# Kernel optimization log

Hardware: AMD Instinct MI355X
Metric: run time of the kernel (lower is better)

## Reference

```python
import jax, jax.numpy as jnp
import numpy as np

B, N, D, H = 16, 512, 256, 8
DK = D // H
EPS = 1e-6
NEG_INF = 1e12
LAM_ATT, LAM_DIST, LAM_ADJ = 0.3, 0.3, 0.4


def setup_inputs() -> dict:
    key = jax.random.key(0)
    ks = jax.random.split(key, 16)
    inp = {
        "query": jax.random.normal(ks[0], (B, N, D), jnp.float32),
        "key": jax.random.normal(ks[1], (B, N, D), jnp.float32),
        "value": jax.random.normal(ks[2], (B, N, D), jnp.float32),
        "adj_matrix": jax.random.uniform(ks[3], (B, N, N), jnp.float32),
        "distances_matrix": jax.random.uniform(ks[4], (B, N, N), jnp.float32),
        "edges_att": jnp.zeros((1,), jnp.float32),
        "mask": jnp.ones((B, N), jnp.int32),
    }
    s = 1.0 / np.sqrt(D)
    # four Linear(d_model, d_model): Wq, Wk, Wv, Wo (+ biases)
    for i, nm in enumerate(["q", "k", "v", "o"]):
        inp[f"W{nm}"] = jax.random.normal(ks[5 + 2 * i], (D, D), jnp.float32) * s
        inp[f"b{nm}"] = jax.random.normal(ks[6 + 2 * i], (D,), jnp.float32) * s
    return inp


def _proj(x, W, b):
    # [B,N,D] -> [B,H,N,DK]
    y = x @ W.T + b
    return y.reshape(B, N, H, DK).transpose(0, 2, 1, 3)


def reference(query, key, value, adj_matrix, distances_matrix, edges_att, mask,
              Wq, bq, Wk, bk, Wv, bv, Wo, bo):
    q = _proj(query, Wq, bq)
    k = _proj(key, Wk, bk)
    v = _proj(value, Wv, bv)

    valid = mask != 0  # [B,N] key-side validity

    # distance kernel: softmax(-d) over keys, masked positions -> 0 prob
    d_scores = jnp.where(valid[:, None, :], -distances_matrix, -jnp.inf)
    p_dist = jax.nn.softmax(d_scores, axis=-1)  # [B,N,N]

    # scaled dot-product attention with key mask
    scores = jnp.einsum("bhqd,bhkd->bhqk", q, k) / np.sqrt(DK)
    scores = jnp.where(valid[:, None, None, :], scores, -NEG_INF)
    p_attn = jax.nn.softmax(scores, axis=-1)  # [B,H,N,N]

    # row-normalized adjacency
    p_adj = adj_matrix / (adj_matrix.sum(axis=-1, keepdims=True) + EPS)  # [B,N,N]

    # blend three attention terms (broadcast dist/adj over heads)
    p_weighted = (LAM_ATT * p_attn
                  + LAM_DIST * p_dist[:, None]
                  + LAM_ADJ * p_adj[:, None])  # [B,H,N,N]

    x = jnp.einsum("bhqk,bhkd->bhqd", p_weighted, v)  # [B,H,N,DK]
    x = x.transpose(0, 2, 1, 3).reshape(B, N, D)
    out = x @ Wo.T + bo  # output projection (4th linear)
    return out
```

## Files before the change

### kernel.cpp

```cpp
#include <hip/hip_runtime.h>
#include <cstdint>
#include <cstddef>

#define B_  16
#define N_  512
#define D_  256
#define H_  8
#define DK_ 32

#define QKV_ELEMS 2097152

__device__ __align__(16) unsigned short g_Qb[QKV_ELEMS];
__device__ __align__(16) unsigned short g_Kb[QKV_ELEMS];
__device__ __align__(16) unsigned short g_VT[QKV_ELEMS];
__device__ __align__(16) unsigned short g_WqB[D_*D_];
__device__ __align__(16) unsigned short g_WkB[D_*D_];
__device__ __align__(16) unsigned short g_WvB[D_*D_];
__device__ __align__(16) unsigned short g_WoB[D_*D_];
__device__ __align__(16) unsigned short g_ST[B_*N_*N_];

typedef short v8s __attribute__((ext_vector_type(8)));
typedef float v4f __attribute__((ext_vector_type(4)));

__device__ __forceinline__ unsigned short f2b(float f){
  unsigned int x;
  __builtin_memcpy(&x, &f, 4);
  x = x + 0x7FFFu + ((x >> 16) & 1u);
  return (unsigned short)(x >> 16);
}
__device__ __forceinline__ v8s pack8(const float4 a, const float4 b){
  v8s o;
  o[0]=(short)f2b(a.x); o[1]=(short)f2b(a.y); o[2]=(short)f2b(a.z); o[3]=(short)f2b(a.w);
  o[4]=(short)f2b(b.x); o[5]=(short)f2b(b.y); o[6]=(short)f2b(b.z); o[7]=(short)f2b(b.w);
  return o;
}

__global__ __launch_bounds__(256) void prep_w(
    const float* __restrict__ Wq, const float* __restrict__ Wk,
    const float* __restrict__ Wv, const float* __restrict__ Wo)
{
  const int bid = blockIdx.x;
  const int z = bid >> 6;
  const int i = ((bid & 63)*256 + (int)threadIdx.x)*4;
  const float* src = (z==0)?Wq:(z==1)?Wk:(z==2)?Wv:Wo;
  const float4 u = *reinterpret_cast<const float4*>(src + i);
  ushort4 o4;
  o4.x = f2b(u.x); o4.y = f2b(u.y); o4.z = f2b(u.z); o4.w = f2b(u.w);
  if (z < 3){
    unsigned short* dst = (z==0)?g_WqB:(z==1)?g_WkB:g_WvB;
    *reinterpret_cast<ushort4*>(dst + i) = o4;
  } else {
    const int n = i >> 8, k = i & 255;
    *reinterpret_cast<ushort4*>(g_WoB + ((size_t)(k >> 5))*8192 + (size_t)n*32 + (k & 31)) = o4;
  }
}

__global__ __launch_bounds__(512) void qkv_st_kernel(
    const float* __restrict__ query, const float* __restrict__ key_,
    const float* __restrict__ value, const float* __restrict__ dist,
    const float* __restrict__ adjm,  const int* __restrict__ mask,
    const float* __restrict__ bq, const float* __restrict__ bk,
    const float* __restrict__ bv)
{
  const int bid = blockIdx.x;
  const int b = bid & 15, qt = bid >> 4, q0 = qt*16;
  const int t = threadIdx.x;
  const int w = t >> 6, lane = t & 63, kl = lane & 15, quad = lane >> 4;

  {
    const int row = t >> 5, seg = t & 31;
    const size_t roff = ((size_t)(b*N_ + q0 + row))*N_ + seg*16;
    const float* dp = dist + roff;
    const float* ap = adjm + roff;
    const int*   mp = mask + b*N_ + seg*16;
    float ev[16], av[16];
    float lz = 0.f, la = 0.f;
    #pragma unroll
    for (int c = 0; c < 4; ++c){
      const float4 d4 = *reinterpret_cast<const float4*>(dp + c*4);
      const float4 a4 = *reinterpret_cast<const float4*>(ap + c*4);
      const int4   m4 = *reinterpret_cast<const int4*>(mp + c*4);
      ev[c*4+0] = m4.x ? __expf(-d4.x) : 0.f;
      ev[c*4+1] = m4.y ? __expf(-d4.y) : 0.f;
      ev[c*4+2] = m4.z ? __expf(-d4.z) : 0.f;
      ev[c*4+3] = m4.w ? __expf(-d4.w) : 0.f;
      av[c*4+0]=a4.x; av[c*4+1]=a4.y; av[c*4+2]=a4.z; av[c*4+3]=a4.w;
      lz += ev[c*4+0]+ev[c*4+1]+ev[c*4+2]+ev[c*4+3];
      la += a4.x+a4.y+a4.z+a4.w;
    }
    #pragma unroll
    for (int o = 1; o < 32; o <<= 1){
      lz += __shfl_xor(lz, o, 64);
      la += __shfl_xor(la, o, 64);
    }
    const float c0 = (lz > 0.f) ? 0.3f / lz : 0.f;
    const float c1 = 0.4f / (la + 1e-6f);
    v8s s0, s1;
    #pragma unroll
    for (int i = 0; i < 8; ++i){
      s0[i] = (short)f2b(ev[i]*c0   + av[i]*c1);
      s1[i] = (short)f2b(ev[8+i]*c0 + av[8+i]*c1);
    }
    *reinterpret_cast<v8s*>(g_ST + roff)     = s0;
    *reinterpret_cast<v8s*>(g_ST + roff + 8) = s1;
  }

  {
    const size_t arow = ((size_t)(b*N_ + q0 + kl))*256;
    const int n0 = w*32;
    const v4f vz = {0.f,0.f,0.f,0.f};
    #pragma unroll
    for (int z = 0; z < 3; ++z){
      const float* Ap = (z==0)?query:(z==1)?key_:value;
      const unsigned short* WB = (z==0)?g_WqB:(z==1)?g_WkB:g_WvB;
      const float* bp = (z==0)?bq:(z==1)?bk:bv;
      v4f a0 = vz, a1 = vz;
      #pragma unroll
      for (int k0 = 0; k0 < 256; k0 += 32){
        const float* app = Ap + arow + k0 + quad*8;
        const v8s af = pack8(reinterpret_cast<const float4*>(app)[0],
                             reinterpret_cast<const float4*>(app)[1]);
        const v8s wf0 = *reinterpret_cast<const v8s*>(WB + ((size_t)(n0+kl))*256 + k0 + quad*8);
        const v8s wf1 = *reinterpret_cast<const v8s*>(WB + ((size_t)(n0+16+kl))*256 + k0 + quad*8);
        if (z < 2){
          a0 = __builtin_amdgcn_mfma_f32_16x16x32_bf16(wf0, af, a0, 0, 0, 0);
          a1 = __builtin_amdgcn_mfma_f32_16x16x32_bf16(wf1, af, a1, 0, 0, 0);
        } else {
          a0 = __builtin_amdgcn_mfma_f32_16x16x32_bf16(af, wf0, a0, 0, 0, 0);
          a1 = __builtin_amdgcn_mfma_f32_16x16x32_bf16(af, wf1, a1, 0, 0, 0);
        }
      }
      if (z < 2){
        unsigned short* dst = (z==0) ? g_Qb : g_Kb;
        #pragma unroll
        for (int nb = 0; nb < 2; ++nb){
          const v4f a = nb ? a1 : a0;
          const int nn = n0 + nb*16 + quad*4;
          const float4 b4 = *reinterpret_cast<const float4*>(bp + nn);
          ushort4 o4;
          o4.x=f2b(a[0]+b4.x); o4.y=f2b(a[1]+b4.y); o4.z=f2b(a[2]+b4.z); o4.w=f2b(a[3]+b4.w);
          *reinterpret_cast<ushort4*>(dst + (((size_t)(b*H_+w))*N_ + q0 + kl)*DK_ + (nn & 31)) = o4;
        }
      } else {
        #pragma unroll
        for (int nb = 0; nb < 2; ++nb){
          const v4f a = nb ? a1 : a0;
          const float bias = bp[n0 + nb*16 + kl];
          ushort4 o4;
          o4.x=f2b(a[0]+bias); o4.y=f2b(a[1]+bias); o4.z=f2b(a[2]+bias); o4.w=f2b(a[3]+bias);
          *reinterpret_cast<ushort4*>(g_VT + (((size_t)(b*H_+w))*16 + (qt>>1))*1024
              + (size_t)(nb*16+kl)*32 + (qt&1)*16 + quad*4) = o4;
        }
      }
    }
  }
}

__global__ __launch_bounds__(512, 4) void attn_kernel(
    const int* __restrict__ mask, const float* __restrict__ bo,
    float* __restrict__ out)
{
  __shared__ unsigned short STl[16*520];
  __shared__ unsigned short Pl[8*16*40];
  __shared__ unsigned short Xl[16*272];
  const int bid = blockIdx.x;
  const int b  = bid & 15;
  const int qt = bid >> 4;
  const int q0 = qt*16;
  const int t  = threadIdx.x;
  const int w  = t >> 6, lane = t & 63;
  const int kl = lane & 15, quad = lane >> 4;

  {
    const int row = t >> 5;
    const int c16 = (t & 31) * 16;
    const unsigned short* src = g_ST + ((size_t)(b*N_ + q0 + row))*N_ + c16;
    *reinterpret_cast<v8s*>(&STl[row*520 + c16])     = *reinterpret_cast<const v8s*>(src);
    *reinterpret_cast<v8s*>(&STl[row*520 + c16 + 8]) = *reinterpret_cast<const v8s*>(src + 8);
  }

  const int h = w;
  const size_t bh = (size_t)b*H_ + h;
  const float scale = 0.17677669529663687f;
  const unsigned short* Qp = g_Qb + (bh*N_ + q0)*DK_;
  const unsigned short* Kp = g_Kb + bh*N_*DK_;
  const unsigned short* Vp = g_VT + bh*(size_t)(N_*DK_);
  unsigned short* Plw = Pl + w*640;
  const int* mrow = mask + b*N_;
  const v8s aq = *reinterpret_cast<const v8s*>(Qp + (size_t)kl*DK_ + quad*8);
  const v4f vz = {0.f, 0.f, 0.f, 0.f};

  v4f oA0 = vz, oA1 = vz;
  v4f oS0 = vz, oS1 = vz;
  float lsum[4] = {0.f, 0.f, 0.f, 0.f};

  __syncthreads();

  #pragma unroll 1
  for (int ch = 0; ch < 4; ++ch){
    const int k0 = ch*128;
    v4f acc[8];
    #pragma unroll
    for (int kb = 0; kb < 8; ++kb){
      const v8s bk = *reinterpret_cast<const v8s*>(Kp + (size_t)(k0 + kb*16 + kl)*DK_ + quad*8);
      acc[kb] = __builtin_amdgcn_mfma_f32_16x16x32_bf16(aq, bk, vz, 0, 0, 0);
    }
    #pragma unroll
    for (int kb = 0; kb < 8; ++kb){
      const bool valid = (mrow[k0 + kb*16 + kl] != 0);
      #pragma unroll
      for (int r = 0; r < 4; ++r){
        const float e = valid ? __expf(acc[kb][r]*scale) : 0.f;
        acc[kb][r] = e;
        lsum[r] += e;
      }
    }
    #pragma unroll
    for (int cc = 0; cc < 4; ++cc){
      #pragma unroll
      for (int r = 0; r < 4; ++r){
        Plw[(quad*4 + r)*40 + kl]      = f2b(acc[2*cc    ][r]);
        Plw[(quad*4 + r)*40 + 16 + kl] = f2b(acc[2*cc + 1][r]);
      }
      const int kk = k0 + cc*32;
      const v8s bp  = *reinterpret_cast<const v8s*>(&Plw[kl*40 + quad*8]);
      const v8s bst = *reinterpret_cast<const v8s*>(&STl[kl*520 + kk + quad*8]);
      const v8s av0 = *reinterpret_cast<const v8s*>(Vp + (size_t)(kk + kl)*32 + quad*8);
      const v8s av1 = *reinterpret_cast<const v8s*>(Vp + (size_t)(kk + 16 + kl)*32 + quad*8);
      oA0 = __builtin_amdgcn_mfma_f32_16x16x32_bf16(av0, bp,  oA0, 0, 0, 0);
      oS0 = __builtin_amdgcn_mfma_f32_16x16x32_bf16(av0, bst, oS0, 0, 0, 0);
      oA1 = __builtin_amdgcn_mfma_f32_16x16x32_bf16(av1, bp,  oA1, 0, 0, 0);
      oS1 = __builtin_amdgcn_mfma_f32_16x16x32_bf16(av1, bst, oS1, 0, 0, 0);
    }
  }

  #pragma unroll
  for (int r = 0; r < 4; ++r)
    #pragma unroll
    for (int o = 1; o < 16; o <<= 1) lsum[r] += __shfl_xor(lsum[r], o, 64);
  const float s01 = (kl & 1) ? lsum[1] : lsum[0];
  const float s23 = (kl & 1) ? lsum[3] : lsum[2];
  const float sv  = (kl & 2) ? s23 : s01;
  float inv = __shfl(sv, ((kl >> 2) << 4) | (kl & 3), 64);
  inv = (inv > 0.f) ? 0.3f / inv : 0.f;

  unsigned short* xr = Xl + kl*272 + h*32;
  #pragma unroll
  for (int r = 0; r < 4; ++r){
    xr[     quad*4 + r] = f2b(oA0[r]*inv + oS0[r]);
    xr[16 + quad*4 + r] = f2b(oA1[r]*inv + oS1[r]);
  }
  __syncthreads();

  {
    const int n0 = w*32;
    v4f a2[2];
    a2[0] = vz; a2[1] = vz;
    #pragma unroll
    for (int k0 = 0; k0 < 256; k0 += 32){
      const v8s af = *reinterpret_cast<const v8s*>(&Xl[kl*272 + k0 + quad*8]);
      #pragma unroll
      for (int nb = 0; nb < 2; ++nb){
        const v8s wf = *reinterpret_cast<const v8s*>(
            g_WoB + (size_t)(k0 >> 5)*8192 + (size_t)(n0 + nb*16 + kl)*32 + quad*8);
        a2[nb] = __builtin_amdgcn_mfma_f32_16x16x32_bf16(af, wf, a2[nb], 0, 0, 0);
      }
    }
    #pragma unroll
    for (int nb = 0; nb < 2; ++nb){
      const int n = n0 + nb*16 + kl;
      const float bias = bo[n];
      #pragma unroll
      for (int r = 0; r < 4; ++r)
        out[((size_t)(b*N_ + q0 + quad*4 + r))*256 + n] = a2[nb][r] + bias;
    }
  }
}

extern "C" void kernel_launch(void* const* d_in, const int* in_sizes, int n_in,
                              void* d_out, int out_size, void* d_ws, size_t ws_size,
                              hipStream_t stream)
{
  const float* query = (const float*)d_in[0];
  const float* key_  = (const float*)d_in[1];
  const float* value = (const float*)d_in[2];
  const float* adjm  = (const float*)d_in[3];
  const float* dist  = (const float*)d_in[4];
  const int*   mask  = (const int*)d_in[6];
  const float* Wq = (const float*)d_in[7];  const float* bq = (const float*)d_in[8];
  const float* Wk = (const float*)d_in[9];  const float* bk = (const float*)d_in[10];
  const float* Wv = (const float*)d_in[11]; const float* bv = (const float*)d_in[12];
  const float* Wo = (const float*)d_in[13]; const float* bo = (const float*)d_in[14];

  prep_w<<<256, 256, 0, stream>>>(Wq, Wk, Wv, Wo);
  qkv_st_kernel<<<512, 512, 0, stream>>>(query, key_, value, dist, adjm, mask,
                                         bq, bk, bv);
  attn_kernel<<<512, 512, 0, stream>>>(mask, bo, (float*)d_out);
}
```

Before: 190.1 us.

## Split pre-kernel into separate ST and QKV projection blocks with interleaved loads

The combined kernel is split so even blocks compute the blended distance/adjacency matrix and odd blocks compute the Q/K/V projections, doubling the grid to 1024 blocks. The projection loop now issues all Q, K and V loads up front per k-step and runs six independent MFMA chains instead of three sequential passes. The ST path also hoists all its global loads before the exp work. The aim is more parallelism and memory-level overlap, at the cost of higher register pressure per thread in the projection path.

```diff
diff --git a/kernel.cpp b/kernel.cpp
--- a/kernel.cpp
+++ b/kernel.cpp
@@ -55,7 +55,7 @@
   }
 }
 
-__global__ __launch_bounds__(512) void qkv_st_kernel(
+__global__ __launch_bounds__(512, 4) void pre_kernel(
     const float* __restrict__ query, const float* __restrict__ key_,
     const float* __restrict__ value, const float* __restrict__ dist,
     const float* __restrict__ adjm,  const int* __restrict__ mask,
@@ -63,31 +63,45 @@
     const float* __restrict__ bv)
 {
   const int bid = blockIdx.x;
-  const int b = bid & 15, qt = bid >> 4, q0 = qt*16;
-  const int t = threadIdx.x;
-  const int w = t >> 6, lane = t & 63, kl = lane & 15, quad = lane >> 4;
-
-  {
+  const int role = bid & 1;
+  const int b  = (bid >> 1) & 15;
+  const int qt = bid >> 5;
+  const int q0 = qt*16;
+  const int t  = threadIdx.x;
+
+  if (role == 0){
     const int row = t >> 5, seg = t & 31;
     const size_t roff = ((size_t)(b*N_ + q0 + row))*N_ + seg*16;
     const float* dp = dist + roff;
     const float* ap = adjm + roff;
     const int*   mp = mask + b*N_ + seg*16;
+    const float4 d0 = reinterpret_cast<const float4*>(dp)[0];
+    const float4 d1 = reinterpret_cast<const float4*>(dp)[1];
+    const float4 d2 = reinterpret_cast<const float4*>(dp)[2];
+    const float4 d3 = reinterpret_cast<const float4*>(dp)[3];
+    const float4 a0 = reinterpret_cast<const float4*>(ap)[0];
+    const float4 a1 = reinterpret_cast<const float4*>(ap)[1];
+    const float4 a2 = reinterpret_cast<const float4*>(ap)[2];
+    const float4 a3 = reinterpret_cast<const float4*>(ap)[3];
+    const int4   m0 = reinterpret_cast<const int4*>(mp)[0];
+    const int4   m1 = reinterpret_cast<const int4*>(mp)[1];
+    const int4   m2 = reinterpret_cast<const int4*>(mp)[2];
+    const int4   m3 = reinterpret_cast<const int4*>(mp)[3];
+
     float ev[16], av[16];
+    #define ST_STEP(i, d4, a4, m4) \
+      ev[i+0] = m4.x ? __expf(-d4.x) : 0.f;  av[i+0] = a4.x; \
+      ev[i+1] = m4.y ? __expf(-d4.y) : 0.f;  av[i+1] = a4.y; \
+      ev[i+2] = m4.z ? __expf(-d4.z) : 0.f;  av[i+2] = a4.z; \
+      ev[i+3] = m4.w ? __expf(-d4.w) : 0.f;  av[i+3] = a4.w;
+    ST_STEP(0,  d0, a0, m0)
+    ST_STEP(4,  d1, a1, m1)
+    ST_STEP(8,  d2, a2, m2)
+    ST_STEP(12, d3, a3, m3)
+    #undef ST_STEP
     float lz = 0.f, la = 0.f;
     #pragma unroll
-    for (int c = 0; c < 4; ++c){
-      const float4 d4 = *reinterpret_cast<const float4*>(dp + c*4);
-      const float4 a4 = *reinterpret_cast<const float4*>(ap + c*4);
-      const int4   m4 = *reinterpret_cast<const int4*>(mp + c*4);
-      ev[c*4+0] = m4.x ? __expf(-d4.x) : 0.f;
-      ev[c*4+1] = m4.y ? __expf(-d4.y) : 0.f;
-      ev[c*4+2] = m4.z ? __expf(-d4.z) : 0.f;
-      ev[c*4+3] = m4.w ? __expf(-d4.w) : 0.f;
-      av[c*4+0]=a4.x; av[c*4+1]=a4.y; av[c*4+2]=a4.z; av[c*4+3]=a4.w;
-      lz += ev[c*4+0]+ev[c*4+1]+ev[c*4+2]+ev[c*4+3];
-      la += a4.x+a4.y+a4.z+a4.w;
-    }
+    for (int i = 0; i < 16; ++i){ lz += ev[i]; la += av[i]; }
     #pragma unroll
     for (int o = 1; o < 32; o <<= 1){
       lz += __shfl_xor(lz, o, 64);
@@ -103,56 +117,73 @@
     }
     *reinterpret_cast<v8s*>(g_ST + roff)     = s0;
     *reinterpret_cast<v8s*>(g_ST + roff + 8) = s1;
-  }
-
-  {
-    const size_t arow = ((size_t)(b*N_ + q0 + kl))*256;
-    const int n0 = w*32;
-    const v4f vz = {0.f,0.f,0.f,0.f};
-    #pragma unroll
-    for (int z = 0; z < 3; ++z){
-      const float* Ap = (z==0)?query:(z==1)?key_:value;
-      const unsigned short* WB = (z==0)?g_WqB:(z==1)?g_WkB:g_WvB;
-      const float* bp = (z==0)?bq:(z==1)?bk:bv;
-      v4f a0 = vz, a1 = vz;
-      #pragma unroll
-      for (int k0 = 0; k0 < 256; k0 += 32){
-        const float* app = Ap + arow + k0 + quad*8;
-        const v8s af = pack8(reinterpret_cast<const float4*>(app)[0],
-                             reinterpret_cast<const float4*>(app)[1]);
-        const v8s wf0 = *reinterpret_cast<const v8s*>(WB + ((size_t)(n0+kl))*256 + k0 + quad*8);
-        const v8s wf1 = *reinterpret_cast<const v8s*>(WB + ((size_t)(n0+16+kl))*256 + k0 + quad*8);
-        if (z < 2){
-          a0 = __builtin_amdgcn_mfma_f32_16x16x32_bf16(wf0, af, a0, 0, 0, 0);
-          a1 = __builtin_amdgcn_mfma_f32_16x16x32_bf16(wf1, af, a1, 0, 0, 0);
-        } else {
-          a0 = __builtin_amdgcn_mfma_f32_16x16x32_bf16(af, wf0, a0, 0, 0, 0);
-          a1 = __builtin_amdgcn_mfma_f32_16x16x32_bf16(af, wf1, a1, 0, 0, 0);
-        }
-      }
-      if (z < 2){
-        unsigned short* dst = (z==0) ? g_Qb : g_Kb;
-        #pragma unroll
-        for (int nb = 0; nb < 2; ++nb){
-          const v4f a = nb ? a1 : a0;
-          const int nn = n0 + nb*16 + quad*4;
-          const float4 b4 = *reinterpret_cast<const float4*>(bp + nn);
-          ushort4 o4;
-          o4.x=f2b(a[0]+b4.x); o4.y=f2b(a[1]+b4.y); o4.z=f2b(a[2]+b4.z); o4.w=f2b(a[3]+b4.w);
-          *reinterpret_cast<ushort4*>(dst + (((size_t)(b*H_+w))*N_ + q0 + kl)*DK_ + (nn & 31)) = o4;
-        }
-      } else {
-        #pragma unroll
-        for (int nb = 0; nb < 2; ++nb){
-          const v4f a = nb ? a1 : a0;
-          const float bias = bp[n0 + nb*16 + kl];
-          ushort4 o4;
-          o4.x=f2b(a[0]+bias); o4.y=f2b(a[1]+bias); o4.z=f2b(a[2]+bias); o4.w=f2b(a[3]+bias);
-          *reinterpret_cast<ushort4*>(g_VT + (((size_t)(b*H_+w))*16 + (qt>>1))*1024
-              + (size_t)(nb*16+kl)*32 + (qt&1)*16 + quad*4) = o4;
-        }
-      }
-    }
+    return;
+  }
+
+  const int w = t >> 6, lane = t & 63, kl = lane & 15, quad = lane >> 4;
+  const size_t arow = ((size_t)(b*N_ + q0 + kl))*256;
+  const int n0 = w*32;
+  const v4f vz = {0.f,0.f,0.f,0.f};
+
+  const float* qp = query + arow;
+  const float* kp = key_  + arow;
+  const float* vp = value + arow;
+  const unsigned short* wq0p = g_WqB + (size_t)(n0      + kl)*256;
+  const unsigned short* wq1p = g_WqB + (size_t)(n0 + 16 + kl)*256;
+  const unsigned short* wk0p = g_WkB + (size_t)(n0      + kl)*256;
+  const unsigned short* wk1p = g_WkB + (size_t)(n0 + 16 + kl)*256;
+  const unsigned short* wv0p = g_WvB + (size_t)(n0      + kl)*256;
+  const unsigned short* wv1p = g_WvB + (size_t)(n0 + 16 + kl)*256;
+
+  v4f cq0 = vz, cq1 = vz, ck0 = vz, ck1 = vz, cv0 = vz, cv1 = vz;
+  #pragma unroll
+  for (int k0 = 0; k0 < 256; k0 += 32){
+    const int o = k0 + quad*8;
+    const float4 qa = *reinterpret_cast<const float4*>(qp + o);
+    const float4 qb = *reinterpret_cast<const float4*>(qp + o + 4);
+    const float4 ka = *reinterpret_cast<const float4*>(kp + o);
+    const float4 kb = *reinterpret_cast<const float4*>(kp + o + 4);
+    const float4 va = *reinterpret_cast<const float4*>(vp + o);
+    const float4 vb = *reinterpret_cast<const float4*>(vp + o + 4);
+    const v8s wq0 = *reinterpret_cast<const v8s*>(wq0p + o);
+    const v8s wq1 = *reinterpret_cast<const v8s*>(wq1p + o);
+    const v8s wk0 = *reinterpret_cast<const v8s*>(wk0p + o);
+    const v8s wk1 = *reinterpret_cast<const v8s*>(wk1p + o);
+    const v8s wv0 = *reinterpret_cast<const v8s*>(wv0p + o);
+    const v8s wv1 = *reinterpret_cast<const v8s*>(wv1p + o);
+    const v8s fq = pack8(qa, qb);
+    const v8s fk = pack8(ka, kb);
+    const v8s fv = pack8(va, vb);
+    cq0 = __builtin_amdgcn_mfma_f32_16x16x32_bf16(wq0, fq, cq0, 0, 0, 0);
+    cq1 = __builtin_amdgcn_mfma_f32_16x16x32_bf16(wq1, fq, cq1, 0, 0, 0);
+    ck0 = __builtin_amdgcn_mfma_f32_16x16x32_bf16(wk0, fk, ck0, 0, 0, 0);
+    ck1 = __builtin_amdgcn_mfma_f32_16x16x32_bf16(wk1, fk, ck1, 0, 0, 0);
+    cv0 = __builtin_amdgcn_mfma_f32_16x16x32_bf16(fv, wv0, cv0, 0, 0, 0);
+    cv1 = __builtin_amdgcn_mfma_f32_16x16x32_bf16(fv, wv1, cv1, 0, 0, 0);
+  }
+
+  #pragma unroll
+  for (int nb = 0; nb < 2; ++nb){
+    const v4f aQ = nb ? cq1 : cq0;
+    const v4f aK = nb ? ck1 : ck0;
+    const int nn = n0 + nb*16 + quad*4;
+    const float4 bq4 = *reinterpret_cast<const float4*>(bq + nn);
+    const float4 bk4 = *reinterpret_cast<const float4*>(bk + nn);
+    ushort4 oq, ok;
+    oq.x=f2b(aQ[0]+bq4.x); oq.y=f2b(aQ[1]+bq4.y); oq.z=f2b(aQ[2]+bq4.z); oq.w=f2b(aQ[3]+bq4.w);
+    ok.x=f2b(aK[0]+bk4.x); ok.y=f2b(aK[1]+bk4.y); ok.z=f2b(aK[2]+bk4.z); ok.w=f2b(aK[3]+bk4.w);
+    const size_t base = (((size_t)(b*H_+w))*N_ + q0 + kl)*DK_ + (nn & 31);
+    *reinterpret_cast<ushort4*>(g_Qb + base) = oq;
+    *reinterpret_cast<ushort4*>(g_Kb + base) = ok;
+  }
+  #pragma unroll
+  for (int nb = 0; nb < 2; ++nb){
+    const v4f aV = nb ? cv1 : cv0;
+    const float bias = bv[n0 + nb*16 + kl];
+    ushort4 ov;
+    ov.x=f2b(aV[0]+bias); ov.y=f2b(aV[1]+bias); ov.z=f2b(aV[2]+bias); ov.w=f2b(aV[3]+bias);
+    *reinterpret_cast<ushort4*>(g_VT + (((size_t)(b*H_+w))*16 + (qt>>1))*1024
+        + (size_t)(nb*16+kl)*32 + (qt&1)*16 + quad*4) = ov;
   }
 }
 
@@ -293,7 +324,7 @@
   const float* Wo = (const float*)d_in[13]; const float* bo = (const float*)d_in[14];
 
   prep_w<<<256, 256, 0, stream>>>(Wq, Wk, Wv, Wo);
-  qkv_st_kernel<<<512, 512, 0, stream>>>(query, key_, value, dist, adjm, mask,
-                                         bq, bk, bv);
+  pre_kernel<<<1024, 512, 0, stream>>>(query, key_, value, dist, adjm, mask,
+                                       bq, bk, bv);
   attn_kernel<<<512, 512, 0, stream>>>(mask, bo, (float*)d_out);
 }
```

Measured after the change: 229.1 us. 1.21x slower.
